# Optimization experiments

Hardware: AMD Instinct MI355X
Metric: run time of the kernel (lower is better)

Reference implementation:

```python
import jax, jax.numpy as jnp
import numpy as np

NEPOCHS = 100  # matches nepochs in init_kwargs


def lstm_cell(x, h, c, W_ih, W_hh, b_ih, b_hh):
    # PyTorch LSTM gate order: i, f, g, o
    gates = x @ W_ih.T + b_ih + h @ W_hh.T + b_hh  # (B, 4H)
    i, f, g, o = jnp.split(gates, 4, axis=-1)
    c_new = jax.nn.sigmoid(f) * c + jax.nn.sigmoid(i) * jnp.tanh(g)
    h_new = jax.nn.sigmoid(o) * jnp.tanh(c_new)
    return h_new, c_new


def setup_inputs() -> dict:
    key = jax.random.key(0)
    T, B, V, H, C = 400, 256, 128, 512, 64
    ks = jax.random.split(key, 8)
    s = 0.05
    return {
        "X": jax.random.normal(ks[0], (T, B, V), dtype=jnp.float32),
        "noise": jax.random.uniform(ks[1], (T, B, C), dtype=jnp.float32),
        "W_ih": jax.random.normal(ks[2], (4 * H, V + C), dtype=jnp.float32) * s,
        "W_hh": jax.random.normal(ks[3], (4 * H, H), dtype=jnp.float32) * s,
        "b_ih": jnp.zeros((4 * H,), jnp.float32),
        "b_hh": jnp.zeros((4 * H,), jnp.float32),
        "W_out": jax.random.normal(ks[4], (C, H), dtype=jnp.float32) * s,
        "b_out": jnp.zeros((C,), jnp.float32),
        "W_ctrl": jax.random.normal(ks[5], (C, H + C + 1), dtype=jnp.float32) * s,
        "b_ctrl": jnp.zeros((C,), jnp.float32),
        "epoch": 5,
    }


def reference(X, noise, W_ih, W_hh, b_ih, b_hh, W_out, b_out, W_ctrl, b_ctrl, epoch):
    T, B, V = X.shape
    C = W_out.shape[0]
    H = W_hh.shape[1]
    sg = jax.lax.stop_gradient
    # epsilon schedule: exp(-linspace(0, 7, nepochs))[epoch]  (training mode)
    eps = jnp.exp(-jnp.linspace(0.0, 7.0, NEPOCHS))[epoch]

    def step(carry, xs):
        h, c, y_bar, preds, halt_pts = carry
        x_t, n_t, t = xs
        # RNN input: raw features || detached halting indicators y_bar
        rnn_in = jnp.concatenate([x_t, sg(y_bar)], axis=-1)  # (B, V+C)
        h, c = lstm_cell(rnn_in, h, c, W_ih, W_hh, b_ih, b_hh)
        y_hat = jax.nn.sigmoid(h @ W_out.T + b_out)  # (B, C)
        time_col = t * jnp.ones((B, 1), X.dtype)
        # controller input is detached
        c_in = sg(jnp.concatenate([h, y_hat, time_col], axis=-1))  # (B, H+C+1)
        probs = jax.nn.sigmoid(c_in @ W_ctrl.T + b_ctrl)
        probs = (1.0 - eps) * probs + eps * 0.05  # explore/exploit smoothing
        a_t = n_t < probs  # Bernoulli sample via supplied uniform noise, (B,C) bool
        preds = jnp.where(a_t & (preds == 0.0), y_hat, preds)
        y_bar = jnp.where(a_t & (y_bar == 0.0), 1.0, y_bar)
        halt_pts = jnp.where((halt_pts == -1.0) & a_t, t, halt_pts)
        return (h, c, y_bar, preds, halt_pts), y_hat

    carry0 = (
        jnp.zeros((B, H), X.dtype),
        jnp.zeros((B, H), X.dtype),
        jnp.zeros((B, C), X.dtype),
        jnp.zeros((B, C), X.dtype),
        -jnp.ones((B, C), X.dtype),
    )
    ts = jnp.arange(T, dtype=X.dtype)
    (h, c, y_bar, preds, halt_pts), all_y = jax.lax.scan(step, carry0, (X, noise, ts))

    # classes never halted fall back to the last prediction
    y_hat_final = jnp.where(preds == 0.0, all_y[-1], preds)  # (B, C)
    halt_pts = jnp.where(halt_pts == -1.0, jnp.asarray(T - 1, X.dtype), halt_pts)
    mean_halting_point = (1.0 + sg(halt_pts)).mean() / (T + 1)
    return y_hat_final, mean_halting_point
```

## Files before the change

kernel.cpp:

```cpp
#include <hip/hip_runtime.h>
#include <math.h>

#define TT 400
#define BBATCH 256
#define VDIM 128
#define CDIM 64
#define HDIM 512
#define NCHUNK 11
#define TSPLIT 160
#define P1B 1024

typedef double d4 __attribute__((ext_vector_type(4)));

__device__ __forceinline__ double sigd(double x) {
  if (x >= 0.0) { double e = exp(-x); return 1.0 / (1.0 + e); }
  double e = exp(x); return e / (1.0 + e);
}

__global__ __launch_bounds__(256) void k_init(
    float* __restrict__ wtro, const float* __restrict__ W_out,
    float* __restrict__ wtrc, const float* __restrict__ W_ctrl,
    int* __restrict__ rowlive, int* __restrict__ alive, int* __restrict__ done)
{
  const int i = blockIdx.x * 256 + threadIdx.x;
  if (i < HDIM * CDIM) {
    const int k = i >> 6, c = i & 63;
    wtro[i] = W_out[c * HDIM + k];
  }
  if (i < 577 * CDIM) {
    const int k = i >> 6, c = i & 63;
    wtrc[i] = W_ctrl[c * 577 + k];
  }
  if (i < BBATCH) rowlive[i] = 1;
  if (i < TT) alive[i] = 0;
  if (i < TT * 16) done[i] = 0;
}


__device__ __forceinline__ void phase1_body(
    const float* __restrict__ X, const float* __restrict__ W_ih,
    const float* __restrict__ W_hh, const float* __restrict__ b_ih,
    const float* __restrict__ b_hh, const double* __restrict__ hR,
    double* __restrict__ hW, double* __restrict__ cst,
    const double* __restrict__ ybar, int t, int cb, int rb, int tid,
    double (*aF)[2][8][66], float (*bF)[2][2][8][68])
{
  const int lane = tid & 63;
  const int wid  = tid >> 6;
  const int r0   = rb * 16;
  const int hbase = cb * 8;

  double* gsp = &aF[0][0][0][0];

  const int sA  = tid & 7;
  const int khA = (tid >> 3) & 1;
  const int rrA = tid >> 4;

  int rowm[4], colm[4];
  {
    d4 dp = {0.0, 0.0, 0.0, 0.0};
    const double ap = (lane < 16) ? (double)(lane + 1) : (lane < 32 ? 1.0 : 0.0);
    const double bp = (lane < 16) ? 1.0
                    : (lane < 32 ? 1000.0 * (double)((lane & 15) + 1) : 0.0);
    dp = __builtin_amdgcn_mfma_f64_16x16x4f64(ap, bp, dp, 0, 0, 0);
    #pragma unroll
    for (int r = 0; r < 4; ++r) {
      const int iv = (int)(dp[r] + 0.5);
      rowm[r] = ((iv % 1000) - 1) & 15;
      colm[r] = ((iv / 1000) - 1) & 15;
    }
  }

  double pa[4];
  float4 pw0, pw1;
  const int c0 = rrA, c1 = 16 + rrA;
  const int wg0 = (c0 >> 3) * HDIM + hbase + (c0 & 7);
  const int wg1 = (c1 >> 3) * HDIM + hbase + (c1 & 7);

  auto load_to = [&](int ci) {
    const int kk = ci * 64 + khA * 32 + sA * 4;
    const int rr = r0 + rrA;
    if (kk < VDIM) {
      const float4 v = *(const float4*)(X + ((size_t)t * BBATCH + rr) * VDIM + kk);
      pa[0] = v.x; pa[1] = v.y; pa[2] = v.z; pa[3] = v.w;
    } else if (t == 0) {
      pa[0] = 0.0; pa[1] = 0.0; pa[2] = 0.0; pa[3] = 0.0;
    } else if (kk < VDIM + CDIM) {
      const double2 v0 = *(const double2*)(ybar + (size_t)rr * CDIM + (kk - VDIM));
      const double2 v1 = *(const double2*)(ybar + (size_t)rr * CDIM + (kk - VDIM) + 2);
      pa[0] = v0.x; pa[1] = v0.y; pa[2] = v1.x; pa[3] = v1.y;
    } else {
      const double2 v0 = *(const double2*)(hR + (size_t)rr * HDIM + (kk - 192));
      const double2 v1 = *(const double2*)(hR + (size_t)rr * HDIM + (kk - 192) + 2);
      pa[0] = v0.x; pa[1] = v0.y; pa[2] = v1.x; pa[3] = v1.y;
    }
    pw0 = (kk < 192) ? *(const float4*)(W_ih + (size_t)wg0 * 192 + kk)
                     : *(const float4*)(W_hh + (size_t)wg0 * HDIM + (kk - 192));
    pw1 = (kk < 192) ? *(const float4*)(W_ih + (size_t)wg1 * 192 + kk)
                     : *(const float4*)(W_hh + (size_t)wg1 * HDIM + (kk - 192));
  };
  auto store_to = [&](int buf) {
    #pragma unroll
    for (int j = 0; j < 4; ++j)
      aF[buf][khA][sA][16 * j + rrA] = pa[j];
    *(float4*)&bF[buf][khA][0][sA][rrA * 4] = pw0;
    *(float4*)&bF[buf][khA][1][sA][rrA * 4] = pw1;
  };

  const int ct = wid & 1, kh = wid >> 1;
  d4 aa = {0.0, 0.0, 0.0, 0.0}, ab = aa;

  load_to(0);
  store_to(0);
  __syncthreads();

  for (int ci = 0; ci < NCHUNK; ++ci) {
    const int p = ci & 1;
    if (ci + 1 < NCHUNK) load_to(ci + 1);
    #pragma unroll
    for (int ss = 0; ss < 8; ++ss) {
      const double av = aF[p][kh][ss][lane];
      const double bv = (double)bF[p][kh][ct][ss][(lane & 15) * 4 + (lane >> 4)];
      if (ss & 1) ab = __builtin_amdgcn_mfma_f64_16x16x4f64(av, bv, ab, 0, 0, 0);
      else        aa = __builtin_amdgcn_mfma_f64_16x16x4f64(av, bv, aa, 0, 0, 0);
    }
    if (ci + 1 < NCHUNK) store_to(p ^ 1);
    __syncthreads();
  }
  const d4 acc = aa + ab;

  #pragma unroll
  for (int r = 0; r < 4; ++r)
    gsp[kh * 528 + rowm[r] * 33 + 16 * ct + colm[r]] = acc[r];
  __syncthreads();

  if (tid < 128) {
    const int jj = tid & 7, r = tid >> 3;
    const int g0 = hbase + jj;
    const double gi = gsp[r * 33 + jj]      + gsp[528 + r * 33 + jj]
                    + (double)b_ih[0 * HDIM + g0] + (double)b_hh[0 * HDIM + g0];
    const double gf = gsp[r * 33 + 8 + jj]  + gsp[528 + r * 33 + 8 + jj]
                    + (double)b_ih[1 * HDIM + g0] + (double)b_hh[1 * HDIM + g0];
    const double gg = gsp[r * 33 + 16 + jj] + gsp[528 + r * 33 + 16 + jj]
                    + (double)b_ih[2 * HDIM + g0] + (double)b_hh[2 * HDIM + g0];
    const double go = gsp[r * 33 + 24 + jj] + gsp[528 + r * 33 + 24 + jj]
                    + (double)b_ih[3 * HDIM + g0] + (double)b_hh[3 * HDIM + g0];
    const size_t oidx = (size_t)(r0 + r) * HDIM + g0;
    const double cold = (t == 0) ? 0.0 : cst[oidx];
    const double cn = sigd(gf) * cold + sigd(gi) * tanh(gg);
    const double hn = sigd(go) * tanh(cn);
    cst[oidx] = cn;
    hW[oidx]  = hn;
  }
}

__device__ __forceinline__ void phase2_body(
    const double* __restrict__ h, const float* __restrict__ wtro,
    const float* __restrict__ b_out, const float* __restrict__ wtrc,
    const float* __restrict__ b_ctrl, const float* __restrict__ noise,
    const int* __restrict__ epoch_p, double* __restrict__ ybar,
    double* __restrict__ preds, float* __restrict__ halt,
    double* __restrict__ ylast, int* __restrict__ rowlive,
    int* __restrict__ alive, int t, int b, int tid, double* sh)
{
  double* hsh = sh;
  double* p1  = hsh + HDIM;
  double* p2  = p1 + 256;
  double* ysh = p2 + 256;

  *(double2*)&hsh[2 * tid] = *(const double2*)(h + (size_t)b * HDIM + 2 * tid);
  __syncthreads();

  const int c = tid & 63, kq = tid >> 6;
  const int k0 = kq * 128;

  double s1 = 0.0, s2 = 0.0;
  #pragma unroll 8
  for (int k = k0; k < k0 + 128; ++k) {
    const double hk = hsh[k];
    s1 += hk * (double)wtro[k * 64 + c];
    s2 += hk * (double)wtrc[k * 64 + c];
  }
  p1[kq * 64 + c] = s1;
  p2[kq * 64 + c] = s2;
  __syncthreads();

  if (tid < 64)
    ysh[tid] = sigd(p1[tid] + p1[64 + tid] + p1[128 + tid] + p1[192 + tid]
                    + (double)b_out[tid]);
  __syncthreads();

  if (tid < 64) {
    double a2 = p2[tid] + p2[64 + tid] + p2[128 + tid] + p2[192 + tid];
    #pragma unroll 8
    for (int j = 0; j < CDIM; ++j)
      a2 += ysh[j] * (double)wtrc[(512 + j) * 64 + tid];
    a2 += (double)t * (double)wtrc[576 * 64 + tid] + (double)b_ctrl[tid];

    const double eps = exp(-7.0 * (double)(*epoch_p) / 99.0);
    const double pr  = (1.0 - eps) * sigd(a2) + eps * 0.05;
    const double n   = (double)noise[((size_t)t * BBATCH + b) * CDIM + tid];
    const bool   at  = n < pr;
    const double yh  = ysh[tid];
    const size_t i   = (size_t)b * CDIM + tid;

    const double pred_old = (t == 0) ? 0.0  : preds[i];
    const double ybar_old = (t == 0) ? 0.0  : ybar[i];
    const float  halt_old = (t == 0) ? -1.0f : halt[i];

    const double pred_new = (at && pred_old == 0.0) ? yh : pred_old;
    preds[i] = pred_new;
    ybar[i]  = (at && ybar_old == 0.0) ? 1.0 : ybar_old;
    halt[i]  = (halt_old == -1.0f && at) ? (float)t : halt_old;
    ylast[i] = yh;

    const unsigned long long m = __ballot(pred_new == 0.0);
    if (tid == 0) {
      rowlive[b] = (m != 0ull) ? 1 : 0;
      if (m != 0ull) atomicOr(alive + t, 1);
    }
  }
}


__global__ __launch_bounds__(256, 4) void k_phase1(
    const float* __restrict__ X, const float* __restrict__ W_ih,
    const float* __restrict__ W_hh, const float* __restrict__ b_ih,
    const float* __restrict__ b_hh, const double* __restrict__ hR,
    double* __restrict__ hW, double* __restrict__ cst,
    const double* __restrict__ ybar, const int* __restrict__ rowlive,
    const int* __restrict__ alive, int t)
{
  if (t > 0 && alive[t - 1] == 0) return;
  const int tid = threadIdx.x, lane = tid & 63;
  const int cb = blockIdx.x, rb = blockIdx.y;
  if (t > 0) {
    const unsigned long long m =
        __ballot((lane < 16) && (rowlive[rb * 16 + (lane & 15)] != 0));
    if (m == 0ull) return;
  }
  __shared__ __align__(16) double aF[2][2][8][66];
  __shared__ __align__(16) float  bF[2][2][2][8][68];
  phase1_body(X, W_ih, W_hh, b_ih, b_hh, hR, hW, cst, ybar, t, cb, rb, tid, aF, bF);
}

__global__ __launch_bounds__(256) void k_phase2(
    const double* __restrict__ h, const float* __restrict__ wtro,
    const float* __restrict__ b_out, const float* __restrict__ wtrc,
    const float* __restrict__ b_ctrl, const float* __restrict__ noise,
    const int* __restrict__ epoch_p, double* __restrict__ ybar,
    double* __restrict__ preds, float* __restrict__ halt,
    double* __restrict__ ylast, int* __restrict__ rowlive,
    int* __restrict__ alive, int t)
{
  const int tid = threadIdx.x;
  const int b   = blockIdx.x;
  if (t > 0 && rowlive[b] == 0) return;
  __shared__ double sh[HDIM + 256 + 256 + 64];
  phase2_body(h, wtro, b_out, wtrc, b_ctrl, noise, epoch_p, ybar, preds, halt,
              ylast, rowlive, alive, t, b, tid, sh);
}


__global__ __launch_bounds__(256, 4) void k_tail(
    const float* __restrict__ X, const float* __restrict__ W_ih,
    const float* __restrict__ W_hh, const float* __restrict__ b_ih,
    const float* __restrict__ b_hh, const float* __restrict__ wtro,
    const float* __restrict__ b_out, const float* __restrict__ wtrc,
    const float* __restrict__ b_ctrl, const float* __restrict__ noise,
    const int* __restrict__ epoch_p, const double* __restrict__ hR,
    double* __restrict__ hW, double* __restrict__ cst,
    double* __restrict__ ybar, double* __restrict__ preds,
    float* __restrict__ halt, double* __restrict__ ylast,
    int* __restrict__ rowlive, int* __restrict__ alive,
    int* __restrict__ done, int t)
{
  if (alive[t - 1] == 0) return;

  const int tid  = threadIdx.x;
  const int lane = tid & 63;
  const int bid  = blockIdx.x;

  __shared__ __align__(16) double aF[2][2][8][66];
  __shared__ __align__(16) float  bF[2][2][2][8][68];

  if (bid < P1B) {
    const int cb = bid & 63, rb = bid >> 6;
    const unsigned long long m =
        __ballot((lane < 16) && (rowlive[rb * 16 + (lane & 15)] != 0));
    if (m == 0ull) {
      if (tid == 0) atomicAdd(&done[t * 16 + rb], 1);
      return;
    }
    phase1_body(X, W_ih, W_hh, b_ih, b_hh, hR, hW, cst, ybar, t, cb, rb, tid, aF, bF);
    __syncthreads();
    if (tid == 0) {
      __threadfence();
      atomicAdd(&done[t * 16 + rb], 1);
    }
  } else {
    const int b = bid - P1B;
    if (rowlive[b] == 0) return;
    if (tid == 0) {
      while (__hip_atomic_load(&done[t * 16 + (b >> 4)], __ATOMIC_ACQUIRE,
                               __HIP_MEMORY_SCOPE_AGENT) < 64)
        __builtin_amdgcn_s_sleep(8);
      __threadfence();
    }
    __syncthreads();
    phase2_body(hW, wtro, b_out, wtrc, b_ctrl, noise, epoch_p, ybar, preds, halt,
                ylast, rowlive, alive, t, b, tid, &aF[0][0][0][0]);
  }
}

__global__ __launch_bounds__(256) void k_final_out(
    const double* __restrict__ preds, const double* __restrict__ ylast,
    float* __restrict__ out)
{
  const int i = blockIdx.x * 256 + threadIdx.x;
  const double p = preds[i];
  out[i] = (float)(p == 0.0 ? ylast[i] : p);
}

__global__ __launch_bounds__(256) void k_final_mean(
    const float* __restrict__ halt, float* __restrict__ out)
{
  __shared__ double s[256];
  double acc = 0.0;
  for (int i = threadIdx.x; i < BBATCH * CDIM; i += 256) {
    const float hp = halt[i];
    acc += 1.0 + (hp == -1.0f ? (double)(TT - 1) : (double)hp);
  }
  s[threadIdx.x] = acc;
  __syncthreads();
  for (int off = 128; off > 0; off >>= 1) {
    if (threadIdx.x < off) s[threadIdx.x] += s[threadIdx.x + off];
    __syncthreads();
  }
  if (threadIdx.x == 0)
    out[BBATCH * CDIM] = (float)(s[0] / (double)(BBATCH * CDIM) / (double)(TT + 1));
}

extern "C" void kernel_launch(void* const* d_in, const int* in_sizes, int n_in,
                              void* d_out, int out_size, void* d_ws, size_t ws_size,
                              hipStream_t stream)
{
  const float* X      = (const float*)d_in[0];
  const float* noise  = (const float*)d_in[1];
  const float* W_ih   = (const float*)d_in[2];
  const float* W_hh   = (const float*)d_in[3];
  const float* b_ih   = (const float*)d_in[4];
  const float* b_hh   = (const float*)d_in[5];
  const float* W_out  = (const float*)d_in[6];
  const float* b_out  = (const float*)d_in[7];
  const float* W_ctrl = (const float*)d_in[8];
  const float* b_ctrl = (const float*)d_in[9];
  const int*   epoch  = (const int*)d_in[10];
  float* out = (float*)d_out;

  char* ws = (char*)d_ws;
  double* h0      = (double*)ws;
  double* h1      = h0    + (size_t)BBATCH * HDIM;
  double* cst     = h1    + (size_t)BBATCH * HDIM;
  double* ybar    = cst   + (size_t)BBATCH * HDIM;
  double* preds   = ybar  + (size_t)BBATCH * CDIM;
  double* ylast   = preds + (size_t)BBATCH * CDIM;
  float*  halt    = (float*)(ylast + (size_t)BBATCH * CDIM);
  float*  wtro    = halt + (size_t)BBATCH * CDIM;
  float*  wtrc    = wtro + (size_t)HDIM * CDIM;
  int*    rowlive = (int*)(wtrc + (size_t)577 * CDIM);
  int*    alive   = rowlive + BBATCH;
  int*    done    = alive + TT;

  k_init<<<145, 256, 0, stream>>>(wtro, W_out, wtrc, W_ctrl, rowlive, alive, done);

  for (int t = 0; t < TT; ++t) {
    const double* hR = (t & 1) ? h1 : h0;
    double*       hW = (t & 1) ? h0 : h1;
    if (t < TSPLIT) {
      k_phase1<<<dim3(64, 16), 256, 0, stream>>>(X, W_ih, W_hh, b_ih, b_hh,
                                                 hR, hW, cst, ybar, rowlive, alive, t);
      k_phase2<<<BBATCH, 256, 0, stream>>>(hW, wtro, b_out, wtrc, b_ctrl, noise,
                                           epoch, ybar, preds, halt, ylast,
                                           rowlive, alive, t);
    } else {
      k_tail<<<P1B + BBATCH, 256, 0, stream>>>(
          X, W_ih, W_hh, b_ih, b_hh, wtro, b_out, wtrc, b_ctrl, noise, epoch,
          hR, hW, cst, ybar, preds, halt, ylast, rowlive, alive, done, t);
    }
  }

  k_final_out<<<64, 256, 0, stream>>>(preds, ylast, out);
  k_final_mean<<<1, 256, 0, stream>>>(halt, out);
}
```

Before: 3.880 ms.

## Fuse phase2 of step t-1 into phase1 of step t with ybar-chunk wait

```diff
diff --git a/kernel.cpp b/kernel.cpp
--- a/kernel.cpp
+++ b/kernel.cpp
@@ -7,8 +7,6 @@
 #define CDIM 64
 #define HDIM 512
 #define NCHUNK 11
-#define TSPLIT 160
-#define P1B 1024
 
 typedef double d4 __attribute__((ext_vector_type(4)));
 
@@ -32,8 +30,7 @@
     wtrc[i] = W_ctrl[c * 577 + k];
   }
   if (i < BBATCH) rowlive[i] = 1;
-  if (i < TT) alive[i] = 0;
-  if (i < TT * 16) done[i] = 0;
+  if (i < TT) { alive[i] = 0; done[i] = 0; }
 }
 
 
@@ -42,7 +39,8 @@
     const float* __restrict__ W_hh, const float* __restrict__ b_ih,
     const float* __restrict__ b_hh, const double* __restrict__ hR,
     double* __restrict__ hW, double* __restrict__ cst,
-    const double* __restrict__ ybar, int t, int cb, int rb, int tid,
+    const double* __restrict__ ybar, const int* __restrict__ wait_flag,
+    int t, int cb, int rb, int tid,
     double (*aF)[2][8][66], float (*bF)[2][2][8][68])
 {
   const int lane = tid & 63;
@@ -110,13 +108,26 @@
   const int ct = wid & 1, kh = wid >> 1;
   d4 aa = {0.0, 0.0, 0.0, 0.0}, ab = aa;
 
-  load_to(0);
+  const int seq[NCHUNK] = {0, 1, 3, 4, 5, 6, 7, 8, 9, 10, 2};
+
+  load_to(seq[0]);
   store_to(0);
   __syncthreads();
 
-  for (int ci = 0; ci < NCHUNK; ++ci) {
-    const int p = ci & 1;
-    if (ci + 1 < NCHUNK) load_to(ci + 1);
+  for (int pos = 0; pos < NCHUNK; ++pos) {
+    const int p = pos & 1;
+    if (pos + 1 < NCHUNK) {
+      if (pos + 1 == NCHUNK - 1 && wait_flag) {
+        if (tid == 0) {
+          while (__hip_atomic_load(wait_flag, __ATOMIC_ACQUIRE,
+                                   __HIP_MEMORY_SCOPE_AGENT) < BBATCH)
+            __builtin_amdgcn_s_sleep(2);
+          __threadfence();
+        }
+        __syncthreads();
+      }
+      load_to(seq[pos + 1]);
+    }
     #pragma unroll
     for (int ss = 0; ss < 8; ++ss) {
       const double av = aF[p][kh][ss][lane];
@@ -124,7 +135,7 @@
       if (ss & 1) ab = __builtin_amdgcn_mfma_f64_16x16x4f64(av, bv, ab, 0, 0, 0);
       else        aa = __builtin_amdgcn_mfma_f64_16x16x4f64(av, bv, aa, 0, 0, 0);
     }
-    if (ci + 1 < NCHUNK) store_to(p ^ 1);
+    if (pos + 1 < NCHUNK) store_to(p ^ 1);
     __syncthreads();
   }
   const d4 acc = aa + ab;
@@ -222,47 +233,7 @@
   }
 }
 
-
-__global__ __launch_bounds__(256, 4) void k_phase1(
-    const float* __restrict__ X, const float* __restrict__ W_ih,
-    const float* __restrict__ W_hh, const float* __restrict__ b_ih,
-    const float* __restrict__ b_hh, const double* __restrict__ hR,
-    double* __restrict__ hW, double* __restrict__ cst,
-    const double* __restrict__ ybar, const int* __restrict__ rowlive,
-    const int* __restrict__ alive, int t)
-{
-  if (t > 0 && alive[t - 1] == 0) return;
-  const int tid = threadIdx.x, lane = tid & 63;
-  const int cb = blockIdx.x, rb = blockIdx.y;
-  if (t > 0) {
-    const unsigned long long m =
-        __ballot((lane < 16) && (rowlive[rb * 16 + (lane & 15)] != 0));
-    if (m == 0ull) return;
-  }
-  __shared__ __align__(16) double aF[2][2][8][66];
-  __shared__ __align__(16) float  bF[2][2][2][8][68];
-  phase1_body(X, W_ih, W_hh, b_ih, b_hh, hR, hW, cst, ybar, t, cb, rb, tid, aF, bF);
-}
-
-__global__ __launch_bounds__(256) void k_phase2(
-    const double* __restrict__ h, const float* __restrict__ wtro,
-    const float* __restrict__ b_out, const float* __restrict__ wtrc,
-    const float* __restrict__ b_ctrl, const float* __restrict__ noise,
-    const int* __restrict__ epoch_p, double* __restrict__ ybar,
-    double* __restrict__ preds, float* __restrict__ halt,
-    double* __restrict__ ylast, int* __restrict__ rowlive,
-    int* __restrict__ alive, int t)
-{
-  const int tid = threadIdx.x;
-  const int b   = blockIdx.x;
-  if (t > 0 && rowlive[b] == 0) return;
-  __shared__ double sh[HDIM + 256 + 256 + 64];
-  phase2_body(h, wtro, b_out, wtrc, b_ctrl, noise, epoch_p, ybar, preds, halt,
-              ylast, rowlive, alive, t, b, tid, sh);
-}
-
-
-__global__ __launch_bounds__(256, 4) void k_tail(
+__global__ __launch_bounds__(256, 4) void k_stepm(
     const float* __restrict__ X, const float* __restrict__ W_ih,
     const float* __restrict__ W_hh, const float* __restrict__ b_ih,
     const float* __restrict__ b_hh, const float* __restrict__ wtro,
@@ -275,42 +246,53 @@
     int* __restrict__ rowlive, int* __restrict__ alive,
     int* __restrict__ done, int t)
 {
-  if (alive[t - 1] == 0) return;
-
   const int tid  = threadIdx.x;
   const int lane = tid & 63;
   const int bid  = blockIdx.x;
 
+  if (t > 1 && alive[t - 2] == 0) return;
+
   __shared__ __align__(16) double aF[2][2][8][66];
   __shared__ __align__(16) float  bF[2][2][2][8][68];
 
-  if (bid < P1B) {
-    const int cb = bid & 63, rb = bid >> 6;
-    const unsigned long long m =
-        __ballot((lane < 16) && (rowlive[rb * 16 + (lane & 15)] != 0));
-    if (m == 0ull) {
-      if (tid == 0) atomicAdd(&done[t * 16 + rb], 1);
-      return;
-    }
-    phase1_body(X, W_ih, W_hh, b_ih, b_hh, hR, hW, cst, ybar, t, cb, rb, tid, aF, bF);
+  if (t > 0 && bid < BBATCH) {
+    if (rowlive[bid] != 0)
+      phase2_body(hR, wtro, b_out, wtrc, b_ctrl, noise, epoch_p, ybar, preds,
+                  halt, ylast, rowlive, alive, t - 1, bid, tid, &aF[0][0][0][0]);
     __syncthreads();
     if (tid == 0) {
       __threadfence();
-      atomicAdd(&done[t * 16 + rb], 1);
-    }
-  } else {
-    const int b = bid - P1B;
-    if (rowlive[b] == 0) return;
-    if (tid == 0) {
-      while (__hip_atomic_load(&done[t * 16 + (b >> 4)], __ATOMIC_ACQUIRE,
-                               __HIP_MEMORY_SCOPE_AGENT) < 64)
-        __builtin_amdgcn_s_sleep(8);
-      __threadfence();
+      atomicAdd(&done[t - 1], 1);
     }
     __syncthreads();
-    phase2_body(hW, wtro, b_out, wtrc, b_ctrl, noise, epoch_p, ybar, preds, halt,
-                ylast, rowlive, alive, t, b, tid, &aF[0][0][0][0]);
-  }
+  }
+
+  const int cb = bid & 63;
+  const int rb = bid >> 6;
+  if (t > 0) {
+    const unsigned long long m =
+        __ballot((lane < 16) && (rowlive[rb * 16 + (lane & 15)] != 0));
+    if (m == 0ull) return;
+  }
+  phase1_body(X, W_ih, W_hh, b_ih, b_hh, hR, hW, cst, ybar,
+              (t > 0) ? &done[t - 1] : nullptr, t, cb, rb, tid, aF, bF);
+}
+
+__global__ __launch_bounds__(256) void k_phase2(
+    const double* __restrict__ h, const float* __restrict__ wtro,
+    const float* __restrict__ b_out, const float* __restrict__ wtrc,
+    const float* __restrict__ b_ctrl, const float* __restrict__ noise,
+    const int* __restrict__ epoch_p, double* __restrict__ ybar,
+    double* __restrict__ preds, float* __restrict__ halt,
+    double* __restrict__ ylast, int* __restrict__ rowlive,
+    int* __restrict__ alive, int t)
+{
+  const int tid = threadIdx.x;
+  const int b   = blockIdx.x;
+  if (t > 0 && rowlive[b] == 0) return;
+  __shared__ double sh[HDIM + 256 + 256 + 64];
+  phase2_body(h, wtro, b_out, wtrc, b_ctrl, noise, epoch_p, ybar, preds, halt,
+              ylast, rowlive, alive, t, b, tid, sh);
 }
 
 __global__ __launch_bounds__(256) void k_final_out(
@@ -377,17 +359,15 @@
   for (int t = 0; t < TT; ++t) {
     const double* hR = (t & 1) ? h1 : h0;
     double*       hW = (t & 1) ? h0 : h1;
-    if (t < TSPLIT) {
-      k_phase1<<<dim3(64, 16), 256, 0, stream>>>(X, W_ih, W_hh, b_ih, b_hh,
-                                                 hR, hW, cst, ybar, rowlive, alive, t);
-      k_phase2<<<BBATCH, 256, 0, stream>>>(hW, wtro, b_out, wtrc, b_ctrl, noise,
-                                           epoch, ybar, preds, halt, ylast,
-                                           rowlive, alive, t);
-    } else {
-      k_tail<<<P1B + BBATCH, 256, 0, stream>>>(
-          X, W_ih, W_hh, b_ih, b_hh, wtro, b_out, wtrc, b_ctrl, noise, epoch,
-          hR, hW, cst, ybar, preds, halt, ylast, rowlive, alive, done, t);
-    }
+    k_stepm<<<1024, 256, 0, stream>>>(
+        X, W_ih, W_hh, b_ih, b_hh, wtro, b_out, wtrc, b_ctrl, noise, epoch,
+        hR, hW, cst, ybar, preds, halt, ylast, rowlive, alive, done, t);
+  }
+  {
+    double* hW = ((TT - 1) & 1) ? h0 : h1;
+    k_phase2<<<BBATCH, 256, 0, stream>>>(hW, wtro, b_out, wtrc, b_ctrl, noise,
+                                         epoch, ybar, preds, halt, ylast,
+                                         rowlive, alive, TT - 1);
   }
 
   k_final_out<<<64, 256, 0, stream>>>(preds, ylast, out);
```

After: 8.329 ms. 2.15x slower.

## Replace per-step tail kernel launches with one persistent cooperative kernel using grid sync

Applied to the files above, without the earlier changes.

```diff
diff --git a/kernel.cpp b/kernel.cpp
--- a/kernel.cpp
+++ b/kernel.cpp
@@ -1,4 +1,5 @@
 #include <hip/hip_runtime.h>
+#include <hip/hip_cooperative_groups.h>
 #include <math.h>
 
 #define TT 400
@@ -8,7 +9,8 @@
 #define HDIM 512
 #define NCHUNK 11
 #define TSPLIT 160
-#define P1B 1024
+
+namespace cg = cooperative_groups;
 
 typedef double d4 __attribute__((ext_vector_type(4)));
 
@@ -20,7 +22,7 @@
 __global__ __launch_bounds__(256) void k_init(
     float* __restrict__ wtro, const float* __restrict__ W_out,
     float* __restrict__ wtrc, const float* __restrict__ W_ctrl,
-    int* __restrict__ rowlive, int* __restrict__ alive, int* __restrict__ done)
+    int* __restrict__ rowlive, int* __restrict__ alive)
 {
   const int i = blockIdx.x * 256 + threadIdx.x;
   if (i < HDIM * CDIM) {
@@ -33,7 +35,6 @@
   }
   if (i < BBATCH) rowlive[i] = 1;
   if (i < TT) alive[i] = 0;
-  if (i < TT * 16) done[i] = 0;
 }
 
 
@@ -261,22 +262,19 @@
               ylast, rowlive, alive, t, b, tid, sh);
 }
 
-
-__global__ __launch_bounds__(256, 4) void k_tail(
+__global__ __launch_bounds__(256, 4) void k_tailloop(
     const float* __restrict__ X, const float* __restrict__ W_ih,
     const float* __restrict__ W_hh, const float* __restrict__ b_ih,
     const float* __restrict__ b_hh, const float* __restrict__ wtro,
     const float* __restrict__ b_out, const float* __restrict__ wtrc,
     const float* __restrict__ b_ctrl, const float* __restrict__ noise,
-    const int* __restrict__ epoch_p, const double* __restrict__ hR,
-    double* __restrict__ hW, double* __restrict__ cst,
+    const int* __restrict__ epoch_p, double* __restrict__ h0buf,
+    double* __restrict__ h1buf, double* __restrict__ cst,
     double* __restrict__ ybar, double* __restrict__ preds,
     float* __restrict__ halt, double* __restrict__ ylast,
-    int* __restrict__ rowlive, int* __restrict__ alive,
-    int* __restrict__ done, int t)
-{
-  if (alive[t - 1] == 0) return;
-
+    int* __restrict__ rowlive, int* __restrict__ alive)
+{
+  cg::grid_group grid = cg::this_grid();
   const int tid  = threadIdx.x;
   const int lane = tid & 63;
   const int bid  = blockIdx.x;
@@ -284,32 +282,26 @@
   __shared__ __align__(16) double aF[2][2][8][66];
   __shared__ __align__(16) float  bF[2][2][2][8][68];
 
-  if (bid < P1B) {
+  for (int t = TSPLIT; t < TT; ++t) {
+    if (__hip_atomic_load(&alive[t - 1], __ATOMIC_ACQUIRE,
+                          __HIP_MEMORY_SCOPE_AGENT) == 0)
+      return;
+
+    const double* hR = (t & 1) ? h1buf : h0buf;
+    double*       hW = (t & 1) ? h0buf : h1buf;
+
     const int cb = bid & 63, rb = bid >> 6;
     const unsigned long long m =
         __ballot((lane < 16) && (rowlive[rb * 16 + (lane & 15)] != 0));
-    if (m == 0ull) {
-      if (tid == 0) atomicAdd(&done[t * 16 + rb], 1);
-      return;
-    }
-    phase1_body(X, W_ih, W_hh, b_ih, b_hh, hR, hW, cst, ybar, t, cb, rb, tid, aF, bF);
-    __syncthreads();
-    if (tid == 0) {
-      __threadfence();
-      atomicAdd(&done[t * 16 + rb], 1);
-    }
-  } else {
-    const int b = bid - P1B;
-    if (rowlive[b] == 0) return;
-    if (tid == 0) {
-      while (__hip_atomic_load(&done[t * 16 + (b >> 4)], __ATOMIC_ACQUIRE,
-                               __HIP_MEMORY_SCOPE_AGENT) < 64)
-        __builtin_amdgcn_s_sleep(8);
-      __threadfence();
-    }
-    __syncthreads();
-    phase2_body(hW, wtro, b_out, wtrc, b_ctrl, noise, epoch_p, ybar, preds, halt,
-                ylast, rowlive, alive, t, b, tid, &aF[0][0][0][0]);
+    if (m != 0ull)
+      phase1_body(X, W_ih, W_hh, b_ih, b_hh, hR, hW, cst, ybar,
+                  t, cb, rb, tid, aF, bF);
+    grid.sync();
+
+    if (bid < BBATCH && rowlive[bid] != 0)
+      phase2_body(hW, wtro, b_out, wtrc, b_ctrl, noise, epoch_p, ybar, preds,
+                  halt, ylast, rowlive, alive, t, bid, tid, &aF[0][0][0][0]);
+    grid.sync();
   }
 }
 
@@ -370,24 +362,28 @@
   float*  wtrc    = wtro + (size_t)HDIM * CDIM;
   int*    rowlive = (int*)(wtrc + (size_t)577 * CDIM);
   int*    alive   = rowlive + BBATCH;
-  int*    done    = alive + TT;
-
-  k_init<<<145, 256, 0, stream>>>(wtro, W_out, wtrc, W_ctrl, rowlive, alive, done);
-
-  for (int t = 0; t < TT; ++t) {
+
+  k_init<<<145, 256, 0, stream>>>(wtro, W_out, wtrc, W_ctrl, rowlive, alive);
+
+  for (int t = 0; t < TSPLIT; ++t) {
     const double* hR = (t & 1) ? h1 : h0;
     double*       hW = (t & 1) ? h0 : h1;
-    if (t < TSPLIT) {
-      k_phase1<<<dim3(64, 16), 256, 0, stream>>>(X, W_ih, W_hh, b_ih, b_hh,
-                                                 hR, hW, cst, ybar, rowlive, alive, t);
-      k_phase2<<<BBATCH, 256, 0, stream>>>(hW, wtro, b_out, wtrc, b_ctrl, noise,
-                                           epoch, ybar, preds, halt, ylast,
-                                           rowlive, alive, t);
-    } else {
-      k_tail<<<P1B + BBATCH, 256, 0, stream>>>(
-          X, W_ih, W_hh, b_ih, b_hh, wtro, b_out, wtrc, b_ctrl, noise, epoch,
-          hR, hW, cst, ybar, preds, halt, ylast, rowlive, alive, done, t);
-    }
+    k_phase1<<<dim3(64, 16), 256, 0, stream>>>(X, W_ih, W_hh, b_ih, b_hh,
+                                               hR, hW, cst, ybar, rowlive, alive, t);
+    k_phase2<<<BBATCH, 256, 0, stream>>>(hW, wtro, b_out, wtrc, b_ctrl, noise,
+                                         epoch, ybar, preds, halt, ylast,
+                                         rowlive, alive, t);
+  }
+
+  {
+    void* args[] = {
+      (void*)&X, (void*)&W_ih, (void*)&W_hh, (void*)&b_ih, (void*)&b_hh,
+      (void*)&wtro, (void*)&b_out, (void*)&wtrc, (void*)&b_ctrl, (void*)&noise,
+      (void*)&epoch, (void*)&h0, (void*)&h1, (void*)&cst, (void*)&ybar,
+      (void*)&preds, (void*)&halt, (void*)&ylast, (void*)&rowlive, (void*)&alive
+    };
+    hipLaunchCooperativeKernel((const void*)k_tailloop, dim3(1024), dim3(256),
+                               args, 0, stream);
   }
 
   k_final_out<<<64, 256, 0, stream>>>(preds, ylast, out);
```

After: 3.794 ms. 1.02x faster.
